# Optimization experiments

Measured on AMD Instinct MI355X. Metric: run time of the kernel, lower is better.

The kernel has to match this reference:

```python
import jax, jax.numpy as jnp
import numpy as np

N, C, H, W = 128, 3, 256, 256


def setup_inputs() -> dict:
    key = jax.random.key(0)
    k1, k2 = jax.random.split(key)
    inputs = jax.random.normal(k1, (N, C, H, W), dtype=jnp.float32)
    u = jax.random.uniform(k2, (N, 4), dtype=jnp.float32)
    # realistic crop params: scales in (0.3, 1.0], translations in (-0.2, 0.2)
    whbias = jnp.concatenate([0.3 + 0.7 * u[:, :2], 0.4 * u[:, 2:] - 0.2], axis=1)
    return {"inputs": inputs, "whbias": whbias}


def _reflect_clip(x, size):
    # PyTorch grid_sample padding_mode='reflection', align_corners=False:
    # reflect unnormalized coords about [-0.5, size-0.5], then clip to [0, size-1]
    span = float(size)
    x = jnp.abs(x + 0.5) % (2.0 * span)
    x = jnp.where(x > span, 2.0 * span - x, x) - 0.5
    return jnp.clip(x, 0.0, size - 1.0)


def _resized_crop(inputs, whbias):
    n, c, h, w = inputs.shape
    dt = inputs.dtype
    # F.affine_grid base coords, align_corners=False: centers of pixels in [-1, 1]
    xs = (jnp.arange(w, dtype=dt) + 0.5) * (2.0 / w) - 1.0  # [W]
    ys = (jnp.arange(h, dtype=dt) + 0.5) * (2.0 / h) - 1.0  # [H]
    w_s, h_s, w_b, h_b = whbias[:, 0], whbias[:, 1], whbias[:, 2], whbias[:, 3]
    # theta is diagonal + translation -> grid separable in x and y
    gx = w_s[:, None, None] * xs[None, None, :] + w_b[:, None, None]  # [N,H,W]
    gy = h_s[:, None, None] * ys[None, :, None] + h_b[:, None, None]  # [N,H,W]
    # unnormalize (align_corners=False): ix = ((gx+1)*W - 1)/2
    ix = _reflect_clip(((gx + 1.0) * w - 1.0) * 0.5, w)
    iy = _reflect_clip(((gy + 1.0) * h - 1.0) * 0.5, h)
    ix0 = jnp.floor(ix)
    iy0 = jnp.floor(iy)
    wx = (ix - ix0)[:, None]  # [N,1,H,W]
    wy = (iy - iy0)[:, None]
    ix0i = jnp.clip(ix0.astype(jnp.int32), 0, w - 1)
    ix1i = jnp.clip(ix0i + 1, 0, w - 1)
    iy0i = jnp.clip(iy0.astype(jnp.int32), 0, h - 1)
    iy1i = jnp.clip(iy0i + 1, 0, h - 1)

    def gather(img, yy, xx):  # img [C,H,W], yy/xx [H,W] -> [C,H,W]
        return img[:, yy, xx]

    g = jax.vmap(gather)
    v00 = g(inputs, iy0i, ix0i)
    v01 = g(inputs, iy0i, ix1i)
    v10 = g(inputs, iy1i, ix0i)
    v11 = g(inputs, iy1i, ix1i)
    # bilinear blend
    return (v00 * (1.0 - wx) * (1.0 - wy) + v01 * wx * (1.0 - wy)
            + v10 * (1.0 - wx) * wy + v11 * wx * wy)


def reference(inputs, whbias):
    # size=None -> no adaptive_avg_pool2d; output is [N,C,H,W]
    return _resized_crop(inputs, whbias)
```

## Files before the change

kernel.cpp:

```cpp
#include <hip/hip_runtime.h>


constexpr int N_ = 128, C_ = 3, H_ = 256, W_ = 256, HW_ = H_ * W_;
constexpr int ROWS_ = 5;

typedef float f32x4 __attribute__((ext_vector_type(4)));

__device__ __forceinline__ void coord(float scale, float bias, float xf, int size,
                                      int& i0, float& w) {
    const float span = (float)size;
    const float two  = 2.0f * span;
    float xs  = (xf + 0.5f) * (2.0f / span) - 1.0f;
    float g   = scale * xs + bias;
    float pre = ((g + 1.0f) * span - 1.0f) * 0.5f;
    float t = fabsf(pre + 0.5f);
    t = t - two * floorf(t * (1.0f / two));
    t = (t > span) ? (two - t) : t;
    t -= 0.5f;
    t = fminf(fmaxf(t, 0.0f), span - 1.0f);
    float f = floorf(t);
    w  = t - f;
    i0 = (int)f;
}

__global__ __launch_bounds__(256)
void rrc_kernel(const float* __restrict__ in, const float* __restrict__ wh,
                float* __restrict__ out) {
    __shared__ float raw[ROWS_ * W_ + 4];
    __shared__ float Hl[ROWS_ * W_];

    const int n   = blockIdx.x >> 6;
    const int ys  = (blockIdx.x & 63) * 4;
    const int tid = threadIdx.x;
    const int xq  = tid & 63;
    const int yl  = tid >> 6;

    const float w_s = wh[n * 4 + 0];
    const float h_s = wh[n * 4 + 1];
    const float w_b = wh[n * 4 + 2];
    const float h_b = wh[n * 4 + 3];

    int rmin = H_ - 1, rmax = 0;
    int my0 = 0; float wy = 0.0f;
#pragma unroll
    for (int r = 0; r < 4; ++r) {
        int a; float w;
        coord(h_s, h_b, (float)(ys + r), H_, a, w);
        rmin = min(rmin, a);
        rmax = max(rmax, min(a + 1, H_ - 1));
        if (r == yl) { my0 = a; wy = w; }
    }
    const int nrows = rmax - rmin + 1;
    const int words = nrows * 64;
    const int b0 = (my0 - rmin) * W_;
    const int b1 = (min(my0 + 1, H_ - 1) - rmin) * W_;

    const float* __restrict__ inN = in + (size_t)n * C_ * HW_;
    const int r0 = tid >> 6,          sx0 = (tid & 63) * 4;
    const int r1 = (tid + 256) >> 6,  sx1 = sx0;
    const bool m1 = (tid + 256) < words;
    const bool m0 = tid < words;
    f32x4 ga[C_], gb[C_];
#pragma unroll
    for (int c = 0; c < C_; ++c) {
        if (m0) ga[c] = *reinterpret_cast<const f32x4*>(
            inN + c * HW_ + (rmin + r0) * W_ + sx0);
        if (m1) gb[c] = *reinterpret_cast<const f32x4*>(
            inN + c * HW_ + (rmin + r1) * W_ + sx1);
    }

    int hix; float hwx;
    coord(w_s, w_b, (float)tid, W_, hix, hwx);

    float* __restrict__ outN = out + (size_t)n * C_ * HW_;

#pragma unroll
    for (int c = 0; c < C_; ++c) {
        if (m0) *reinterpret_cast<f32x4*>(&raw[r0 * W_ + sx0]) = ga[c];
        if (m1) *reinterpret_cast<f32x4*>(&raw[r1 * W_ + sx1]) = gb[c];
        __syncthreads();
#pragma unroll
        for (int k = 0; k < ROWS_; ++k) {
            const float a = raw[k * W_ + hix];
            const float b = raw[k * W_ + hix + 1];
            Hl[k * W_ + tid] = a + hwx * (b - a);
        }
        __syncthreads();
        const f32x4 h0 = *reinterpret_cast<const f32x4*>(&Hl[b0 + xq * 4]);
        const f32x4 h1 = *reinterpret_cast<const f32x4*>(&Hl[b1 + xq * 4]);
        const f32x4 o  = h0 + wy * (h1 - h0);
        __builtin_nontemporal_store(o, reinterpret_cast<f32x4*>(
            outN + (c * H_ + ys + yl) * W_ + xq * 4));
    }
}

extern "C" void kernel_launch(void* const* d_in, const int* in_sizes, int n_in,
                              void* d_out, int out_size, void* d_ws, size_t ws_size,
                              hipStream_t stream) {
    const float* in = (const float*)d_in[0];
    const float* wh = (const float*)d_in[1];
    float* out      = (float*)d_out;
    (void)in_sizes; (void)n_in; (void)out_size; (void)d_ws; (void)ws_size;

    dim3 grid(N_ * 64);
    dim3 block(256);
    rrc_kernel<<<grid, block, 0, stream>>>(in, wh, out);
}
```

Before: 35.31 us.

## Blend rows vertically first and resample horizontally in per-wave LDS without barriers

The kernel now interpolates the two source rows vertically in registers first. Each 64-lane wave writes its blended row into a private, padded LDS segment and gathers horizontally from it. This removes both block-wide __syncthreads and the shared row-range staging. Padding (one extra word per 32) is meant to cut LDS bank conflicts. In exchange, each wave loads its own two source rows, so the global loads overlap across waves. Correctness also relies on LDS ordering within a wave with no explicit fence, and the output store is no longer nontemporal.

```diff
diff --git a/kernel.cpp b/kernel.cpp
--- a/kernel.cpp
+++ b/kernel.cpp
@@ -2,7 +2,7 @@
 
 
 constexpr int N_ = 128, C_ = 3, H_ = 256, W_ = 256, HW_ = H_ * W_;
-constexpr int ROWS_ = 5;
+constexpr int SEG_ = 264;
 
 typedef float f32x4 __attribute__((ext_vector_type(4)));
 
@@ -26,9 +26,7 @@
 __global__ __launch_bounds__(256)
 void rrc_kernel(const float* __restrict__ in, const float* __restrict__ wh,
                 float* __restrict__ out) {
-    __shared__ float raw[ROWS_ * W_ + 4];
-    __shared__ float Hl[ROWS_ * W_];
-
+    __shared__ float V[4 * C_ * SEG_];
     const int n   = blockIdx.x >> 6;
     const int ys  = (blockIdx.x & 63) * 4;
     const int tid = threadIdx.x;
@@ -40,57 +38,45 @@
     const float w_b = wh[n * 4 + 2];
     const float h_b = wh[n * 4 + 3];
 
-    int rmin = H_ - 1, rmax = 0;
-    int my0 = 0; float wy = 0.0f;
+    int iy0; float wy;
+    coord(h_s, h_b, (float)(ys + yl), H_, iy0, wy);
+    const int iy1 = min(iy0 + 1, H_ - 1);
+
+    int offA[4], offB[4]; float wx[4];
 #pragma unroll
-    for (int r = 0; r < 4; ++r) {
-        int a; float w;
-        coord(h_s, h_b, (float)(ys + r), H_, a, w);
-        rmin = min(rmin, a);
-        rmax = max(rmax, min(a + 1, H_ - 1));
-        if (r == yl) { my0 = a; wy = w; }
+    for (int j = 0; j < 4; ++j) {
+        int i0;
+        coord(w_s, w_b, (float)(xq * 4 + j), W_, i0, wx[j]);
+        const int xb = min(i0 + 1, W_ - 1);
+        offA[j] = i0 + (i0 >> 5);
+        offB[j] = xb + (xb >> 5);
     }
-    const int nrows = rmax - rmin + 1;
-    const int words = nrows * 64;
-    const int b0 = (my0 - rmin) * W_;
-    const int b1 = (min(my0 + 1, H_ - 1) - rmin) * W_;
 
     const float* __restrict__ inN = in + (size_t)n * C_ * HW_;
-    const int r0 = tid >> 6,          sx0 = (tid & 63) * 4;
-    const int r1 = (tid + 256) >> 6,  sx1 = sx0;
-    const bool m1 = (tid + 256) < words;
-    const bool m0 = tid < words;
-    f32x4 ga[C_], gb[C_];
+    f32x4 g0[C_], g1[C_];
 #pragma unroll
     for (int c = 0; c < C_; ++c) {
-        if (m0) ga[c] = *reinterpret_cast<const f32x4*>(
-            inN + c * HW_ + (rmin + r0) * W_ + sx0);
-        if (m1) gb[c] = *reinterpret_cast<const f32x4*>(
-            inN + c * HW_ + (rmin + r1) * W_ + sx1);
+        g0[c] = *reinterpret_cast<const f32x4*>(inN + c * HW_ + iy0 * W_ + xq * 4);
+        g1[c] = *reinterpret_cast<const f32x4*>(inN + c * HW_ + iy1 * W_ + xq * 4);
     }
 
-    int hix; float hwx;
-    coord(w_s, w_b, (float)tid, W_, hix, hwx);
-
     float* __restrict__ outN = out + (size_t)n * C_ * HW_;
+    const int segBase = yl * C_ * SEG_;
+    const int woff    = xq * 4 + (xq >> 3);
 
 #pragma unroll
     for (int c = 0; c < C_; ++c) {
-        if (m0) *reinterpret_cast<f32x4*>(&raw[r0 * W_ + sx0]) = ga[c];
-        if (m1) *reinterpret_cast<f32x4*>(&raw[r1 * W_ + sx1]) = gb[c];
-        __syncthreads();
+        const f32x4 v = g0[c] + wy * (g1[c] - g0[c]);
+        float* seg = &V[segBase + c * SEG_];
+        *reinterpret_cast<f32x4*>(seg + woff) = v;
+        f32x4 o;
 #pragma unroll
-        for (int k = 0; k < ROWS_; ++k) {
-            const float a = raw[k * W_ + hix];
-            const float b = raw[k * W_ + hix + 1];
-            Hl[k * W_ + tid] = a + hwx * (b - a);
+        for (int j = 0; j < 4; ++j) {
+            const float a = seg[offA[j]];
+            const float b = seg[offB[j]];
+            o[j] = a + wx[j] * (b - a);
         }
-        __syncthreads();
-        const f32x4 h0 = *reinterpret_cast<const f32x4*>(&Hl[b0 + xq * 4]);
-        const f32x4 h1 = *reinterpret_cast<const f32x4*>(&Hl[b1 + xq * 4]);
-        const f32x4 o  = h0 + wy * (h1 - h0);
-        __builtin_nontemporal_store(o, reinterpret_cast<f32x4*>(
-            outN + (c * H_ + ys + yl) * W_ + xq * 4));
+        *reinterpret_cast<f32x4*>(outN + (c * H_ + ys + yl) * W_ + xq * 4) = o;
     }
 }
 
```

After: 34.34 us. 1.03x faster.
